# Optimization experiments

Measured on AMD Instinct MI355X. Metric: run time of the kernel, lower is better.

Reference implementation:

```python
import jax, jax.numpy as jnp
import numpy as np

D_MODEL = 512
KEY_DIM = 128
TEMP = 30.0          # RelationUnit temperature
EPS = 1e-5           # InstanceL2Norm eps
SCALE = float(np.sqrt(1.0 / (D_MODEL * 4 * 4)))  # norm_scale in layers


def _sine_pos(hw, d, dtype=jnp.float32):
    # pos_seq = ones(hw).cumsum() -> 1..hw; outer with inv_freq; cat(sin, cos)
    pos = jnp.arange(1, hw + 1, dtype=dtype)
    inv_freq = 1.0 / (10000.0 ** (jnp.arange(0, d, 2, dtype=dtype) / d))
    ang = pos[:, None] * inv_freq[None, :]          # [hw, d/2]
    return jnp.concatenate([jnp.sin(ang), jnp.cos(ang)], axis=-1)  # [hw, d]


def _attn(q, k, v, wk, bk):
    # Single-head RelationUnit: shared WK projection, L2-normalize, temp softmax, raw value.
    # q: [Lq,B,D], k,v: [Lk,B,D]
    pq = q @ wk.T + bk
    pq = pq / jnp.maximum(jnp.linalg.norm(pq, axis=-1, keepdims=True), 1e-12)
    pk = k @ wk.T + bk
    pk = pk / jnp.maximum(jnp.linalg.norm(pk, axis=-1, keepdims=True), 1e-12)
    logits = jnp.einsum('qbe,kbe->bqk', pq, pk) * TEMP   # [B,Lq,Lk]
    a = jax.nn.softmax(logits, axis=-1)
    return jnp.einsum('bqk,kbd->qbd', a, v)


def _inorm(x, ni, b, d, h, w):
    # InstanceL2Norm (size_average=True) over (d,h,w) per (ni,b) sample.
    y = x.reshape(ni, h, w, b, d)
    ss = jnp.sum(y * y, axis=(1, 2, 4), keepdims=True)
    y = y * (SCALE * jnp.sqrt((d * h * w) / (ss + EPS)))
    return y.reshape(ni * h * w, b, d)


def _flatten(x5):
    # (ni,b,d,h,w) -> (ni*h*w, b, d), matching torch view/permute/reshape order.
    ni, b, d, h, w = x5.shape
    return x5.reshape(ni, b, d, h * w).transpose(0, 3, 1, 2).reshape(ni * h * w, b, d)


def _encoder(src5, pos5, wk, bk):
    ni, b, d, h, w = src5.shape
    x = _flatten(src5) + _flatten(pos5) * 1e-3
    x = x + _attn(x, x, x, wk, bk)
    return _inorm(x, ni, b, d, h, w)


def _decoder_one(tgt5, pos5, memory, pos, wk_s, bk_s, wk_c, bk_c):
    # Single decoder layer on one image (ni == 1).
    ni, b, d, h, w = tgt5.shape
    x = _flatten(tgt5) + _flatten(pos5) * 1e-3
    x = x + _attn(x, x, x, wk_s, bk_s)
    x = _inorm(x, ni, b, d, h, w)
    mask = _attn(x, memory, pos, wk_c, bk_c)
    t2 = _inorm(x * mask, ni, b, d, h, w)
    t3 = _attn(x, memory, memory * pos, wk_c, bk_c)
    t4 = _inorm(x + t3, ni, b, d, h, w)
    x = _inorm(t2 + t4, ni, b, d, h, w)
    return x.reshape(ni, h, w, b, d).transpose(0, 3, 4, 1, 2).reshape(ni * b, d, h, w)


def _forward(train_feat, test_feat, train_label, wk_self, bk_self, wk_cross, bk_cross):
    ntr, b, d, h, w = train_feat.shape
    nte = test_feat.shape[0]
    # Sinusoidal position embedding, reshaped to (d,h,w), broadcast over imgs/batch.
    pe = _sine_pos(h * w, d, train_feat.dtype).reshape(h, w, d).transpose(2, 0, 1)
    train_pos = jnp.broadcast_to(pe, (ntr, b, d, h, w))
    test_pos = jnp.broadcast_to(pe, (nte, b, d, h, w))
    memory = _encoder(train_feat, train_pos, wk_self, bk_self)   # [ntr*h*w, b, d]
    # label -> pos value sequence [ntr*h*w, b, d] (repeated over channel dim)
    pos = train_label.reshape(ntr, b, 1, h * w).transpose(0, 3, 1, 2).reshape(ntr * h * w, b, 1)
    pos = jnp.broadcast_to(pos, (ntr * h * w, b, d))

    def dec(t4, p4):
        return _decoder_one(t4[None], p4[None], memory, pos,
                            wk_self, bk_self, wk_cross, bk_cross)

    enc_feat = jax.vmap(dec)(train_feat, train_pos).reshape(ntr * b, d, h, w)
    dec_feat = jax.vmap(dec)(test_feat, test_pos).reshape(nte * b, d, h, w)
    return enc_feat, dec_feat


def setup_inputs() -> dict:
    key = jax.random.key(0)
    k1, k2, k3, k4, k5 = jax.random.split(key, 5)
    NTR, NTE, B, D, H, W = 3, 3, 16, 512, 22, 22
    std = float(np.sqrt(2.0 / D))  # kaiming-like init for WK
    return {
        'train_feat': jax.random.normal(k1, (NTR, B, D, H, W), jnp.float32),
        'test_feat': jax.random.normal(k2, (NTE, B, D, H, W), jnp.float32),
        'train_label': jax.random.uniform(k3, (NTR, B, H, W), jnp.float32),
        'wk_self': jax.random.normal(k4, (KEY_DIM, D), jnp.float32) * std,
        'bk_self': jnp.zeros((KEY_DIM,), jnp.float32),
        'wk_cross': jax.random.normal(k5, (KEY_DIM, D), jnp.float32) * std,
        'bk_cross': jnp.zeros((KEY_DIM,), jnp.float32),
    }


def reference(train_feat, test_feat, train_label, wk_self, bk_self, wk_cross, bk_cross):
    return _forward(train_feat, test_feat, train_label,
                    wk_self, bk_self, wk_cross, bk_cross)
```

## Files before the change

kernel.cpp:

```cpp
#include <hip/hip_runtime.h>
#include <math.h>

#define BATCH   16
#define DMODEL  512
#define EKEY    128
#define HWSZ    484
#define LENC    1452
#define LKPAD   1536
#define IMG_ELEMS (HWSZ*BATCH*DMODEL)
#define ENC_OUT   11894784ull
#define SQRT_TEMP 5.4772255750516611f
#define INORM_SCALE 0.011048543456039806f
#define NEGBIG   -3.0e38f

typedef _Float16 f16;
typedef _Float16 f16x8 __attribute__((ext_vector_type(8)));
typedef _Float16 f16x4 __attribute__((ext_vector_type(4)));
typedef float    f32x4 __attribute__((ext_vector_type(4)));

__device__ __forceinline__ f32x4 mfma16(f16x8 a, f16x8 b, f32x4 c) {
  return __builtin_amdgcn_mfma_f32_16x16x32_f16(a, b, c, 0, 0, 0);
}
__device__ __forceinline__ float inorm_coef(float ss) {
  return INORM_SCALE * sqrtf(247808.0f / (ss + 1e-5f));
}

#define BARRIER() do { asm volatile("s_waitcnt lgkmcnt(0)" ::: "memory"); \
                       __builtin_amdgcn_s_barrier();                      \
                       asm volatile("" ::: "memory"); } while (0)

__global__ void init_zero_kernel(float* __restrict__ ss) { ss[threadIdx.x] = 0.0f; }

__global__ void peT_kernel(float* __restrict__ peT) {
  const int c = blockIdx.x;
  const int cc = (c < 256) ? c : c - 256;
  const float invf = 1.0f / powf(10000.0f, (float)(2 * cc) * (1.0f / 512.0f));
  for (int p = threadIdx.x; p < HWSZ; p += blockDim.x) {
    const float ang = (float)(p + 1) * invf;
    peT[c * HWSZ + p] = (c < 256) ? sinf(ang) : cosf(ang);
  }
}

__global__ void build_labelT_kernel(const float* __restrict__ lab, float* __restrict__ labT) {
  const int g = blockIdx.x;
  if (g < 48) {
    const int im = g >> 4, b = g & 15;
    for (int p = threadIdx.x; p < HWSZ; p += blockDim.x)
      labT[(size_t)b * LKPAD + im * HWSZ + p] = lab[((size_t)im * BATCH + b) * HWSZ + p];
  } else {
    const int b = g - 48;
    for (int p = LENC + threadIdx.x; p < LKPAD; p += blockDim.x)
      labT[(size_t)b * LKPAD + p] = 0.0f;
  }
}

__global__ void cvt16_kernel(const float* __restrict__ s, f16* __restrict__ d) {
  const int i = (blockIdx.x * 256 + threadIdx.x) * 4;
  const float4 v = *(const float4*)(s + i);
  f16x4 h; h[0] = (f16)v.x; h[1] = (f16)v.y; h[2] = (f16)v.z; h[3] = (f16)v.w;
  *(f16x4*)(d + i) = h;
}

__global__ void vpad_kernel(f16* __restrict__ vt) {
  const int d = blockIdx.x, b = blockIdx.y;
  const int c = LENC + threadIdx.x;
  if (c < LKPAD) vt[((size_t)b * 512 + d) * (size_t)LKPAD + c] = (f16)0.f;
}

__global__ __launch_bounds__(256) void build_input_kernel(
    const float* __restrict__ trainf, const float* __restrict__ testf,
    const float* __restrict__ peT, int i0, float* __restrict__ xout,
    f16* __restrict__ vt, int zmul, int col_im_step, int Lkp)
{
  __shared__ float tile[32][33];
  const int tx = threadIdx.x, ty = threadIdx.y;
  const int pt = blockIdx.x * 32, ct = blockIdx.y * 32;
  const int im = blockIdx.z >> 4, b = blockIdx.z & 15;
  const int g = i0 + im;
  const float* src = (g < 3 ? trainf + (size_t)g * IMG_ELEMS
                            : testf + (size_t)(g - 3) * IMG_ELEMS)
                     + (size_t)b * (512 * 484);
  const int zv = zmul ? (im * 16 + b) : b;
  const int col0 = im * col_im_step;
#pragma unroll
  for (int j = 0; j < 4; ++j) {
    const int c = ct + ty + 8 * j, p = pt + tx;
    float val = 0.0f;
    if (p < HWSZ) {
      val = src[(size_t)c * 484 + p] + 1e-3f * peT[(size_t)c * 484 + p];
      vt[((size_t)zv * 512 + c) * (size_t)Lkp + col0 + p] = (f16)val;
    } else if (zmul) {
      vt[((size_t)zv * 512 + c) * (size_t)Lkp + col0 + p] = (f16)0.f;
    }
    tile[ty + 8 * j][tx] = val;
  }
  __syncthreads();
#pragma unroll
  for (int j = 0; j < 4; ++j) {
    const int p = pt + ty + 8 * j, c = ct + tx;
    if (p < HWSZ)
      xout[(((size_t)im * HWSZ + p) * BATCH + b) * DMODEL + c] = tile[tx][ty + 8 * j];
  }
}

__global__ __launch_bounds__(256) void v16t_mem_kernel(
    const float* __restrict__ src, const float* __restrict__ ssE, f16* __restrict__ dst)
{
  __shared__ f16 tile[32][33];
  const int tx = threadIdx.x, ty = threadIdx.y;
  const int l0 = blockIdx.x * 32, d0 = blockIdx.y * 32;
  const int b = blockIdx.z;
#pragma unroll
  for (int j = 0; j < 4; ++j) {
    const int l = l0 + ty + 8 * j;
    float v = 0.0f;
    if (l < LENC) {
      const float cf = inorm_coef(ssE[(l / 484) * 16 + b]);
      v = cf * src[((size_t)l * BATCH + b) * DMODEL + d0 + tx];
    }
    tile[ty + 8 * j][tx] = (f16)v;
  }
  __syncthreads();
#pragma unroll
  for (int j = 0; j < 4; ++j) {
    const int d = d0 + ty + 8 * j, l = l0 + tx;
    if (l < LKPAD) dst[((size_t)b * 512 + d) * (size_t)LKPAD + l] = tile[tx][ty + 8 * j];
  }
}

__global__ __launch_bounds__(256) void proj_mfma_kernel(
    const float* __restrict__ X, const f16* __restrict__ W16,
    const float* __restrict__ bias, const float* __restrict__ ssg,
    f16* __restrict__ P16, int L)
{
  __shared__ f16 Xs[64][72];
  const int t = threadIdx.x;
  const int wave = t >> 6, lane = t & 63, quad = lane >> 4, ln = lane & 15;
  const size_t row0 = (size_t)blockIdx.x * 64;

  f32x4 acc[8];
#pragma unroll
  for (int nt = 0; nt < 8; ++nt) acc[nt] = (f32x4){0.f, 0.f, 0.f, 0.f};

  const int sr = t & 63, sko = (t >> 6) * 16;
  const size_t rowg = row0 + sr;
  float cf = 1.0f;
  if (ssg) {
    const int bb = (int)(rowg & 15);
    const int gg = (int)((rowg >> 4) / 484);
    cf = inorm_coef(ssg[gg * 16 + bb]);
  }
  const float* xp = X + rowg * 512 + sko;

  for (int k0 = 0; k0 < 512; k0 += 64) {
    {
      const float4 a0 = *(const float4*)(xp + k0);
      const float4 a1 = *(const float4*)(xp + k0 + 4);
      const float4 a2 = *(const float4*)(xp + k0 + 8);
      const float4 a3 = *(const float4*)(xp + k0 + 12);
      f16x8 h0, h1;
      h0[0]=(f16)(cf*a0.x); h0[1]=(f16)(cf*a0.y); h0[2]=(f16)(cf*a0.z); h0[3]=(f16)(cf*a0.w);
      h0[4]=(f16)(cf*a1.x); h0[5]=(f16)(cf*a1.y); h0[6]=(f16)(cf*a1.z); h0[7]=(f16)(cf*a1.w);
      h1[0]=(f16)(cf*a2.x); h1[1]=(f16)(cf*a2.y); h1[2]=(f16)(cf*a2.z); h1[3]=(f16)(cf*a2.w);
      h1[4]=(f16)(cf*a3.x); h1[5]=(f16)(cf*a3.y); h1[6]=(f16)(cf*a3.z); h1[7]=(f16)(cf*a3.w);
      *(f16x8*)&Xs[sr][sko]     = h0;
      *(f16x8*)&Xs[sr][sko + 8] = h1;
    }
    __syncthreads();
#pragma unroll
    for (int ks = 0; ks < 2; ++ks) {
      const f16x8 a = *(const f16x8*)&Xs[wave * 16 + ln][ks * 32 + quad * 8];
      const f16* wp = W16 + (size_t)ln * 512 + k0 + ks * 32 + quad * 8;
#pragma unroll
      for (int nt = 0; nt < 8; ++nt) {
        const f16x8 bf = *(const f16x8*)(wp + (size_t)nt * 16 * 512);
        acc[nt] = mfma16(a, bf, acc[nt]);
      }
    }
    __syncthreads();
  }

  float bj[8];
#pragma unroll
  for (int nt = 0; nt < 8; ++nt) bj[nt] = bias[nt * 16 + ln];

  float y[8][4]; float ssq[4] = {0.f, 0.f, 0.f, 0.f};
#pragma unroll
  for (int nt = 0; nt < 8; ++nt)
#pragma unroll
    for (int r = 0; r < 4; ++r) {
      const float v = acc[nt][r] + bj[nt];
      y[nt][r] = v; ssq[r] = fmaf(v, v, ssq[r]);
    }
#pragma unroll
  for (int r = 0; r < 4; ++r) {
    ssq[r] += __shfl_xor(ssq[r], 1); ssq[r] += __shfl_xor(ssq[r], 2);
    ssq[r] += __shfl_xor(ssq[r], 4); ssq[r] += __shfl_xor(ssq[r], 8);
  }
#pragma unroll
  for (int r = 0; r < 4; ++r) {
    const float inv = SQRT_TEMP / fmaxf(sqrtf(ssq[r]), 1e-12f);
    const size_t rg = row0 + (size_t)wave * 16 + quad * 4 + r;
    const int b = (int)(rg & 15);
    const size_t lg = rg >> 4;
    const int im = (int)(lg / (size_t)L);
    const int l  = (int)(lg - (size_t)im * L);
    f16* dp = P16 + ((size_t)(im * 16 + b) * (size_t)L + l) * 128 + ln;
#pragma unroll
    for (int nt = 0; nt < 8; ++nt) dp[nt * 16] = (f16)(y[nt][r] * inv);
  }
}

template<int CROSS>
__global__ __launch_bounds__(512) void attn5_kernel(
    const f16* __restrict__ pq, const f16* __restrict__ pk, const f16* __restrict__ Vt,
    const float* __restrict__ labT, float* __restrict__ X, float* __restrict__ Vout,
    const float* __restrict__ ssIn, float* __restrict__ ssO,
    float* __restrict__ ssV_, float* __restrict__ ssUV_,
    int Lq, int Lk, int Lkp, int nqb, int pk_shared, int vt_shared)
{
  __shared__ float Ssm[64][132];
  __shared__ f16   Psm[64][136];
  __shared__ float msh[64], lsh[64], ash[64], mask_sh[64];

  const int t = threadIdx.x;
  const int wave = t >> 6, lane = t & 63, quad = lane >> 4, ln = lane & 15;

  const int id = blockIdx.x;
  const int b  = (id & 7) + 8 * ((id >> 3) & 1);
  const int jj = id >> 4;
  const int qb = jj % nqb, im = jj / nqb;
  const int q0 = qb * 64;
  const int zq = im * 16 + b;
  const int zk = pk_shared ? b : zq;
  const int zv = vt_shared ? b : zq;

  const f16* pqb = pq + (size_t)zq * Lq * 128;
  const f16* pkb = pk + (size_t)zk * Lk * 128;
  const f16* Vtb = Vt + (size_t)zv * 512 * (size_t)Lkp;
  const float* ksb = CROSS ? labT + (size_t)b * LKPAD : (const float*)0;

  f16x8 qf[4][4];
#pragma unroll
  for (int mt = 0; mt < 4; ++mt) {
    int q = q0 + mt * 16 + ln; if (q > Lq - 1) q = Lq - 1;
    const f16* qp = pqb + (size_t)q * 128 + quad * 8;
#pragma unroll
    for (int es = 0; es < 4; ++es) qf[mt][es] = *(const f16x8*)(qp + es * 32);
  }
  f16x8 kf[4];
  {
    int kn = wave * 16 + ln; if (kn > Lk - 1) kn = Lk - 1;
    const f16* kp = pkb + (size_t)kn * 128 + quad * 8;
#pragma unroll
    for (int es = 0; es < 4; ++es) kf[es] = *(const f16x8*)(kp + es * 32);
  }

  f32x4 oacc[4][4];
#pragma unroll
  for (int mt = 0; mt < 4; ++mt)
#pragma unroll
    for (int nt = 0; nt < 4; ++nt) oacc[mt][nt] = (f32x4){0.f, 0.f, 0.f, 0.f};

  if (t < 64) { msh[t] = NEGBIG; lsh[t] = 0.f; ash[t] = 0.f; }
  float msum = 0.f;
  const int qs = t >> 3, cs = t & 7;
  __syncthreads();

  const f16* vrow = Vtb + (size_t)(wave * 64 + ln) * (size_t)Lkp + quad * 8;
  const int nch = (Lk + 127) >> 7;

  for (int ch = 0; ch < nch; ++ch) {
    const int k0 = ch << 7;
    f16x8 bvA[4], bvB[4];
#pragma unroll
    for (int nt = 0; nt < 4; ++nt) {
      const f16* vpn = vrow + (size_t)nt * 16 * (size_t)Lkp + k0;
      bvA[nt] = *(const f16x8*)(vpn);
      bvB[nt] = *(const f16x8*)(vpn + 32);
    }
    float4 lv[4];
    if (CROSS) {
      const float* lp = ksb + k0 + cs * 16;
#pragma unroll
      for (int i = 0; i < 4; ++i) lv[i] = *(const float4*)(lp + i * 4);
    }
    {
      f32x4 s[4];
#pragma unroll
      for (int mt = 0; mt < 4; ++mt) s[mt] = (f32x4){0.f,0.f,0.f,0.f};
#pragma unroll
      for (int es = 0; es < 4; ++es)
#pragma unroll
        for (int mt = 0; mt < 4; ++mt)
          s[mt] = mfma16(qf[mt][es], kf[es], s[mt]);
#pragma unroll
      for (int mt = 0; mt < 4; ++mt)
#pragma unroll
        for (int r = 0; r < 4; ++r)
          Ssm[mt * 16 + quad * 4 + r][wave * 16 + ln] = s[mt][r];
    }
    if (ch + 1 < nch) {
      int kn = (ch + 1) * 128 + wave * 16 + ln; if (kn > Lk - 1) kn = Lk - 1;
      const f16* kp = pkb + (size_t)kn * 128 + quad * 8;
#pragma unroll
      for (int es = 0; es < 4; ++es) kf[es] = *(const f16x8*)(kp + es * 32);
    }
    BARRIER();
    {
      f32x4 sa[4];
#pragma unroll
      for (int i = 0; i < 4; ++i) sa[i] = *(const f32x4*)&Ssm[qs][cs * 16 + i * 4];
      const int kb = k0 + cs * 16;
      float sv[16];
#pragma unroll
      for (int i = 0; i < 4; ++i)
#pragma unroll
        for (int j = 0; j < 4; ++j)
          sv[i * 4 + j] = (kb + i * 4 + j < Lk) ? sa[i][j] : NEGBIG;
      float mx = sv[0];
#pragma unroll
      for (int j = 1; j < 16; ++j) mx = fmaxf(mx, sv[j]);
      mx = fmaxf(mx, __shfl_xor(mx, 1));
      mx = fmaxf(mx, __shfl_xor(mx, 2));
      mx = fmaxf(mx, __shfl_xor(mx, 4));
      const float mold = msh[qs];
      const float mnew = fmaxf(mold, mx);
      const float alpha = __expf(mold - mnew);
      float ps = 0.f, pm = 0.f;
      f16x8 pv0, pv1;
#pragma unroll
      for (int j = 0; j < 16; ++j) {
        float p = __expf(sv[j] - mnew);
        ps += p;
        if (CROSS) p *= lv[j >> 2][j & 3];
        pm += p;
        if (j < 8) pv0[j] = (f16)p; else pv1[j - 8] = (f16)p;
      }
      *(f16x8*)&Psm[qs][cs * 16]     = pv0;
      *(f16x8*)&Psm[qs][cs * 16 + 8] = pv1;
      ps += __shfl_xor(ps, 1); ps += __shfl_xor(ps, 2); ps += __shfl_xor(ps, 4);
      msum = msum * alpha + pm;
      if (cs == 0) { msh[qs] = mnew; lsh[qs] = lsh[qs] * alpha + ps; ash[qs] = alpha; }
    }
    BARRIER();
    {
      f16x8 bvC[4];
#pragma unroll
      for (int nt = 0; nt < 4; ++nt)
        bvC[nt] = *(const f16x8*)(vrow + (size_t)nt * 16 * (size_t)Lkp + k0 + 64);
#pragma unroll
      for (int mt = 0; mt < 4; ++mt) {
        f32x4 al;
#pragma unroll
        for (int r = 0; r < 4; ++r) al[r] = ash[mt * 16 + quad * 4 + r];
#pragma unroll
        for (int nt = 0; nt < 4; ++nt) oacc[mt][nt] *= al;
      }
      f16x8 pa[4];
#pragma unroll
      for (int mt = 0; mt < 4; ++mt) pa[mt] = *(const f16x8*)&Psm[mt * 16 + ln][quad * 8];
#pragma unroll
      for (int nt = 0; nt < 4; ++nt)
#pragma unroll
        for (int mt = 0; mt < 4; ++mt)
          oacc[mt][nt] = mfma16(pa[mt], bvA[nt], oacc[mt][nt]);
      f16x8 bvD[4];
#pragma unroll
      for (int nt = 0; nt < 4; ++nt)
        bvD[nt] = *(const f16x8*)(vrow + (size_t)nt * 16 * (size_t)Lkp + k0 + 96);
#pragma unroll
      for (int mt = 0; mt < 4; ++mt) pa[mt] = *(const f16x8*)&Psm[mt * 16 + ln][32 + quad * 8];
#pragma unroll
      for (int nt = 0; nt < 4; ++nt)
#pragma unroll
        for (int mt = 0; mt < 4; ++mt)
          oacc[mt][nt] = mfma16(pa[mt], bvB[nt], oacc[mt][nt]);
#pragma unroll
      for (int mt = 0; mt < 4; ++mt) pa[mt] = *(const f16x8*)&Psm[mt * 16 + ln][64 + quad * 8];
#pragma unroll
      for (int nt = 0; nt < 4; ++nt)
#pragma unroll
        for (int mt = 0; mt < 4; ++mt)
          oacc[mt][nt] = mfma16(pa[mt], bvC[nt], oacc[mt][nt]);
#pragma unroll
      for (int mt = 0; mt < 4; ++mt) pa[mt] = *(const f16x8*)&Psm[mt * 16 + ln][96 + quad * 8];
#pragma unroll
      for (int nt = 0; nt < 4; ++nt)
#pragma unroll
        for (int mt = 0; mt < 4; ++mt)
          oacc[mt][nt] = mfma16(pa[mt], bvD[nt], oacc[mt][nt]);
    }
  }

  if (CROSS) {
    float ms = msum;
    ms += __shfl_xor(ms, 1); ms += __shfl_xor(ms, 2); ms += __shfl_xor(ms, 4);
    if (cs == 0) mask_sh[qs] = ms / lsh[qs];
    __syncthreads();
  }

  const int g0  = (im * Lq + q0) / 484;
  const int bhi = (g0 + 1) * 484 - im * Lq;
  const bool strad = (!CROSS) && (bhi < Lq) && (bhi < q0 + 64);

  float a0 = 0.f, a1 = 0.f, a2 = 0.f;
  const float cfA = CROSS ? inorm_coef(ssIn[im * 16 + b]) : 0.f;

#pragma unroll
  for (int mt = 0; mt < 4; ++mt) {
    f32x4 li;
#pragma unroll
    for (int r = 0; r < 4; ++r) li[r] = 1.0f / lsh[mt * 16 + quad * 4 + r];
#pragma unroll
    for (int r = 0; r < 4; ++r) {
      const int q = q0 + mt * 16 + quad * 4 + r;
      if (q < Lq) {
        const size_t base = (((size_t)(im * Lq + q)) * BATCH + b) * DMODEL + wave * 64 + ln;
        if (!CROSS) {
          const bool hi = (q >= bhi);
#pragma unroll
          for (int nt = 0; nt < 4; ++nt) {
            const float y = X[base + nt * 16] + oacc[mt][nt][r] * li[r];
            X[base + nt * 16] = y;
            if (hi) a1 += y * y; else a0 += y * y;
          }
        } else {
          const float mval = mask_sh[mt * 16 + quad * 4 + r];
#pragma unroll
          for (int nt = 0; nt < 4; ++nt) {
            const float x1 = cfA * X[base + nt * 16];
            const float u = x1 * mval;
            const float v = x1 + oacc[mt][nt][r] * li[r];
            X[base + nt * 16] = u;
            Vout[base + nt * 16] = v;
            a0 += u * u; a1 += v * v; a2 += u * v;
          }
        }
      }
    }
  }
#pragma unroll
  for (int m = 32; m; m >>= 1) {
    a0 += __shfl_xor(a0, m); a1 += __shfl_xor(a1, m);
    if (CROSS) a2 += __shfl_xor(a2, m);
  }
  if (lane == 0) {
    if (!CROSS) {
      atomicAdd(ssO + g0 * 16 + b, a0);
      if (strad) atomicAdd(ssO + (g0 + 1) * 16 + b, a1);
    } else {
      const int g = im * 16 + b;
      atomicAdd(ssO + g, a0);
      atomicAdd(ssV_ + g, a1);
      atomicAdd(ssUV_ + g, a2);
    }
  }
}

__global__ void coef_final_kernel(const float* __restrict__ ssU, const float* __restrict__ ssV,
                                  const float* __restrict__ ssUV, float* __restrict__ AB, int n)
{
  const int t = threadIdx.x;
  if (t < n) {
    const float su = ssU[t], sv = ssV[t], suv = ssUV[t];
    const float cu = inorm_coef(su), cv = inorm_coef(sv);
    const float ssz = cu * cu * su + cv * cv * sv + 2.f * cu * cv * suv;
    const float cz = inorm_coef(ssz);
    AB[2 * t] = cu * cz; AB[2 * t + 1] = cv * cz;
  }
}

__global__ __launch_bounds__(256) void final_out_kernel(
    const float* __restrict__ u, const float* __restrict__ v,
    const float* __restrict__ AB, float* __restrict__ out, int i0)
{
  __shared__ float tile[32][33];
  const int tx = threadIdx.x, ty = threadIdx.y;
  const int pt = blockIdx.x * 32, ct = blockIdx.y * 32;
  const int z = blockIdx.z;
  const int im = z >> 4, b = z & 15;
  const float A = AB[2 * z], B = AB[2 * z + 1];
#pragma unroll
  for (int j = 0; j < 4; ++j) {
    const int p = pt + ty + 8 * j, c = ct + tx;
    float val = 0.0f;
    if (p < HWSZ) {
      const size_t idx = (((size_t)im * HWSZ + p) * BATCH + b) * DMODEL + c;
      val = A * u[idx] + B * v[idx];
    }
    tile[ty + 8 * j][tx] = val;
  }
  __syncthreads();
  const int g = i0 + im;
  const size_t base = (g < 3 ? 0ull : ENC_OUT)
                    + ((size_t)(((g < 3 ? g : g - 3) * 16 + b) * 512)) * 484ull;
#pragma unroll
  for (int j = 0; j < 4; ++j) {
    const int c = ct + ty + 8 * j, p = pt + tx;
    if (p < HWSZ) out[base + (size_t)c * 484 + p] = tile[tx][ty + 8 * j];
  }
}

extern "C" void kernel_launch(void* const* d_in, const int* in_sizes, int n_in,
                              void* d_out, int out_size, void* d_ws, size_t ws_size,
                              hipStream_t stream) {
  (void)in_sizes; (void)n_in; (void)out_size;
  const float* train_feat  = (const float*)d_in[0];
  const float* test_feat   = (const float*)d_in[1];
  const float* train_label = (const float*)d_in[2];
  const float* wk_self     = (const float*)d_in[3];
  const float* bk_self     = (const float*)d_in[4];
  const float* wk_cross    = (const float*)d_in[5];
  const float* bk_cross    = (const float*)d_in[6];
  float* out = (float*)d_out;
  char* wsb  = (char*)d_ws;

  size_t off = 0;
  auto alloc = [&](size_t bytes) { size_t r = off; off = (r + bytes + 255) & ~(size_t)255; return r; };
  const size_t o_peT   = alloc(991232ull);
  const size_t o_labT  = alloc(16ull * LKPAD * 4);
  const size_t o_ss    = alloc(4096);
  const size_t o_w16s  = alloc(131072);
  const size_t o_w16c  = alloc(131072);
  const size_t o_xenc  = alloc(47579136ull);
  const size_t o_p16   = alloc(5947392ull);
  const size_t o_vte   = alloc(16ull*512*LKPAD*2);
  const size_t o_vtm   = alloc(16ull*512*LKPAD*2);
  const size_t fixed = off;

  float* peT  = (float*)(wsb + o_peT);
  float* labT = (float*)(wsb + o_labT);
  float* ss   = (float*)(wsb + o_ss);
  f16*   w16s = (f16*)(wsb + o_w16s);
  f16*   w16c = (f16*)(wsb + o_w16c);
  float* xenc = (float*)(wsb + o_xenc);
  f16*   p16  = (f16*)(wsb + o_p16);
  f16*   vte  = (f16*)(wsb + o_vte);
  f16*   vtm  = (f16*)(wsb + o_vtm);
  float* ssE = ss, *ssA = ss + 128, *ssU = ss + 256, *ssV = ss + 384, *ssUV = ss + 512;
  float* AB  = ss + 640;

  const size_t decPer = 15859712ull * 2 + 1982464ull + 8388608ull;
  int NB = 6;
  if (fixed + (size_t)NB * decPer + 4096 > ws_size) NB = 3;
  if (fixed + (size_t)NB * decPer + 4096 > ws_size) NB = 1;

  float* xd    = (float*)(wsb + fixed);
  float* vbuf  = xd + (size_t)NB * IMG_ELEMS;
  f16*   pq16d = (f16*)(vbuf + (size_t)NB * IMG_ELEMS);
  f16*   vtd   = pq16d + (size_t)NB * 991232ull;

  init_zero_kernel<<<dim3(1), dim3(1024), 0, stream>>>(ss);
  peT_kernel<<<dim3(512), dim3(256), 0, stream>>>(peT);
  build_labelT_kernel<<<dim3(64), dim3(256), 0, stream>>>(train_label, labT);
  cvt16_kernel<<<dim3(64), dim3(256), 0, stream>>>(wk_self, w16s);
  cvt16_kernel<<<dim3(64), dim3(256), 0, stream>>>(wk_cross, w16c);
  vpad_kernel<<<dim3(512, 16), dim3(96), 0, stream>>>(vte);

  build_input_kernel<<<dim3(16, 16, 48), dim3(32, 8), 0, stream>>>(
      train_feat, test_feat, peT, 0, xenc, vte, 0, 484, LKPAD);
  proj_mfma_kernel<<<dim3(363), dim3(256), 0, stream>>>(xenc, w16s, bk_self, (const float*)0, p16, LENC);
  attn5_kernel<0><<<dim3(23 * 16), dim3(512), 0, stream>>>(
      p16, p16, vte, (const float*)0, xenc, (float*)0, (const float*)0,
      ssE, (float*)0, (float*)0, LENC, LENC, LKPAD, 23, 0, 0);
  proj_mfma_kernel<<<dim3(363), dim3(256), 0, stream>>>(xenc, w16c, bk_cross, ssE, p16, LENC);
  v16t_mem_kernel<<<dim3(48, 16, 16), dim3(32, 8), 0, stream>>>(xenc, ssE, vtm);

  for (int i0 = 0; i0 < 6; i0 += NB) {
    build_input_kernel<<<dim3(16, 16, NB * 16), dim3(32, 8), 0, stream>>>(
        train_feat, test_feat, peT, i0, xd, vtd, 1, 0, 512);
    proj_mfma_kernel<<<dim3(NB * 121), dim3(256), 0, stream>>>(xd, w16s, bk_self, (const float*)0, pq16d, HWSZ);
    attn5_kernel<0><<<dim3(8 * 16 * NB), dim3(512), 0, stream>>>(
        pq16d, pq16d, vtd, (const float*)0, xd, (float*)0, (const float*)0,
        ssA + i0 * 16, (float*)0, (float*)0, HWSZ, HWSZ, 512, 8, 0, 0);
    proj_mfma_kernel<<<dim3(NB * 121), dim3(256), 0, stream>>>(xd, w16c, bk_cross, ssA + i0 * 16, pq16d, HWSZ);
    attn5_kernel<1><<<dim3(8 * 16 * NB), dim3(512), 0, stream>>>(
        pq16d, p16 , vtm, labT, xd, vbuf, ssA + i0 * 16,
        ssU + i0 * 16, ssV + i0 * 16, ssUV + i0 * 16, HWSZ, LENC, LKPAD, 8, 1, 1);
    coef_final_kernel<<<dim3(1), dim3(128), 0, stream>>>(
        ssU + i0 * 16, ssV + i0 * 16, ssUV + i0 * 16, AB + i0 * 32, NB * 16);
    final_out_kernel<<<dim3(16, 16, NB * 16), dim3(32, 8), 0, stream>>>(
        xd, vbuf, AB + i0 * 32, out, i0);
  }
}
```

Baseline: 1.090 ms.

## Store Q/K/V and weights in MFMA fragment-tiled layout for contiguous lane loads

```diff
diff --git a/kernel.cpp b/kernel.cpp
--- a/kernel.cpp
+++ b/kernel.cpp
@@ -29,6 +29,11 @@
                        __builtin_amdgcn_s_barrier();                      \
                        asm volatile("" ::: "memory"); } while (0)
 
+__device__ __forceinline__ size_t vfrag_addr(size_t z, int nkt, int d, int k) {
+  return (((z * 32 + (d >> 4)) * (size_t)nkt + (k >> 5)) << 9)
+         + (((k >> 3) & 3) << 7) + ((d & 15) << 3) + (k & 7);
+}
+
 __global__ void init_zero_kernel(float* __restrict__ ss) { ss[threadIdx.x] = 0.0f; }
 
 __global__ void peT_kernel(float* __restrict__ peT) {
@@ -56,21 +61,24 @@
 
 __global__ void cvt16_kernel(const float* __restrict__ s, f16* __restrict__ d) {
   const int i = (blockIdx.x * 256 + threadIdx.x) * 4;
+  const int r = i >> 9, c = i & 511;
   const float4 v = *(const float4*)(s + i);
   f16x4 h; h[0] = (f16)v.x; h[1] = (f16)v.y; h[2] = (f16)v.z; h[3] = (f16)v.w;
-  *(f16x4*)(d + i) = h;
+  f16* dp = d + ((((size_t)(r >> 4) << 4) + (c >> 5)) << 9)
+              + (((c >> 3) & 3) << 7) + ((r & 15) << 3) + (c & 7);
+  *(f16x4*)dp = h;
 }
 
 __global__ void vpad_kernel(f16* __restrict__ vt) {
   const int d = blockIdx.x, b = blockIdx.y;
-  const int c = LENC + threadIdx.x;
-  if (c < LKPAD) vt[((size_t)b * 512 + d) * (size_t)LKPAD + c] = (f16)0.f;
+  const int k = LENC + threadIdx.x;
+  if (k < LKPAD) vt[vfrag_addr(b, 48, d, k)] = (f16)0.f;
 }
 
 __global__ __launch_bounds__(256) void build_input_kernel(
     const float* __restrict__ trainf, const float* __restrict__ testf,
     const float* __restrict__ peT, int i0, float* __restrict__ xout,
-    f16* __restrict__ vt, int zmul, int col_im_step, int Lkp)
+    f16* __restrict__ vt, int zmul, int col_im_step, int nkt)
 {
   __shared__ float tile[32][33];
   const int tx = threadIdx.x, ty = threadIdx.y;
@@ -85,12 +93,13 @@
 #pragma unroll
   for (int j = 0; j < 4; ++j) {
     const int c = ct + ty + 8 * j, p = pt + tx;
+    const int k = col0 + p;
     float val = 0.0f;
     if (p < HWSZ) {
       val = src[(size_t)c * 484 + p] + 1e-3f * peT[(size_t)c * 484 + p];
-      vt[((size_t)zv * 512 + c) * (size_t)Lkp + col0 + p] = (f16)val;
+      vt[vfrag_addr(zv, nkt, c, k)] = (f16)val;
     } else if (zmul) {
-      vt[((size_t)zv * 512 + c) * (size_t)Lkp + col0 + p] = (f16)0.f;
+      vt[vfrag_addr(zv, nkt, c, k)] = (f16)0.f;
     }
     tile[ty + 8 * j][tx] = val;
   }
@@ -124,25 +133,26 @@
 #pragma unroll
   for (int j = 0; j < 4; ++j) {
     const int d = d0 + ty + 8 * j, l = l0 + tx;
-    if (l < LKPAD) dst[((size_t)b * 512 + d) * (size_t)LKPAD + l] = tile[tx][ty + 8 * j];
+    if (l < LKPAD) dst[vfrag_addr(b, 48, d, l)] = tile[tx][ty + 8 * j];
   }
 }
 
 __global__ __launch_bounds__(256) void proj_mfma_kernel(
     const float* __restrict__ X, const f16* __restrict__ W16,
     const float* __restrict__ bias, const float* __restrict__ ssg,
-    f16* __restrict__ P16, int L)
+    f16* __restrict__ P16, int L, int NLT)
 {
   __shared__ f16 Xs[64][72];
   const int t = threadIdx.x;
   const int wave = t >> 6, lane = t & 63, quad = lane >> 4, ln = lane & 15;
+  const int lane8 = lane * 8;
   const size_t row0 = (size_t)blockIdx.x * 64;
 
   f32x4 acc[8];
 #pragma unroll
   for (int nt = 0; nt < 8; ++nt) acc[nt] = (f32x4){0.f, 0.f, 0.f, 0.f};
 
-  const int sr = t & 63, sko = (t >> 6) * 16;
+  const int sr = t >> 2, sko = (t & 3) * 16;
   const size_t rowg = row0 + sr;
   float cf = 1.0f;
   if (ssg) {
@@ -170,10 +180,10 @@
 #pragma unroll
     for (int ks = 0; ks < 2; ++ks) {
       const f16x8 a = *(const f16x8*)&Xs[wave * 16 + ln][ks * 32 + quad * 8];
-      const f16* wp = W16 + (size_t)ln * 512 + k0 + ks * 32 + quad * 8;
+      const int kt = (k0 >> 5) + ks;
 #pragma unroll
       for (int nt = 0; nt < 8; ++nt) {
-        const f16x8 bf = *(const f16x8*)(wp + (size_t)nt * 16 * 512);
+        const f16x8 bf = *(const f16x8*)(W16 + (((size_t)(nt * 16 + kt)) << 9) + lane8);
         acc[nt] = mfma16(a, bf, acc[nt]);
       }
     }
@@ -205,19 +215,20 @@
     const size_t lg = rg >> 4;
     const int im = (int)(lg / (size_t)L);
     const int l  = (int)(lg - (size_t)im * L);
-    f16* dp = P16 + ((size_t)(im * 16 + b) * (size_t)L + l) * 128 + ln;
-#pragma unroll
-    for (int nt = 0; nt < 8; ++nt) dp[nt * 16] = (f16)(y[nt][r] * inv);
+    f16* zb = P16 + (((size_t)(im * 16 + b) * NLT + (l >> 4)) << 11) + ((l & 15) << 3) + (ln & 7);
+#pragma unroll
+    for (int nt = 0; nt < 8; ++nt)
+      zb[((size_t)(nt >> 1) << 9) + (((nt * 2 + (ln >> 3)) & 3) << 7)] = (f16)(y[nt][r] * inv);
   }
 }
 
 template<int CROSS>
-__global__ __launch_bounds__(512) void attn5_kernel(
+__global__ __launch_bounds__(512) void attn6_kernel(
     const f16* __restrict__ pq, const f16* __restrict__ pk, const f16* __restrict__ Vt,
     const float* __restrict__ labT, float* __restrict__ X, float* __restrict__ Vout,
     const float* __restrict__ ssIn, float* __restrict__ ssO,
     float* __restrict__ ssV_, float* __restrict__ ssUV_,
-    int Lq, int Lk, int Lkp, int nqb, int pk_shared, int vt_shared)
+    int Lq, int Lk, int nqb, int nltq, int nltk, int nktv, int pk_shared, int vt_shared)
 {
   __shared__ float Ssm[64][132];
   __shared__ f16   Psm[64][136];
@@ -225,6 +236,7 @@
 
   const int t = threadIdx.x;
   const int wave = t >> 6, lane = t & 63, quad = lane >> 4, ln = lane & 15;
+  const int lane8 = lane * 8;
 
   const int id = blockIdx.x;
   const int b  = (id & 7) + 8 * ((id >> 3) & 1);
@@ -235,25 +247,23 @@
   const int zk = pk_shared ? b : zq;
   const int zv = vt_shared ? b : zq;
 
-  const f16* pqb = pq + (size_t)zq * Lq * 128;
-  const f16* pkb = pk + (size_t)zk * Lk * 128;
-  const f16* Vtb = Vt + (size_t)zv * 512 * (size_t)Lkp;
+  const f16* pqz = pq + (((size_t)zq * nltq) << 11);
+  const f16* pkz = pk + (((size_t)zk * nltk) << 11);
+  const f16* Vw  = Vt + ((((size_t)zv * 32 + wave * 4) * (size_t)nktv) << 9) + lane8;
   const float* ksb = CROSS ? labT + (size_t)b * LKPAD : (const float*)0;
 
   f16x8 qf[4][4];
 #pragma unroll
   for (int mt = 0; mt < 4; ++mt) {
-    int q = q0 + mt * 16 + ln; if (q > Lq - 1) q = Lq - 1;
-    const f16* qp = pqb + (size_t)q * 128 + quad * 8;
-#pragma unroll
-    for (int es = 0; es < 4; ++es) qf[mt][es] = *(const f16x8*)(qp + es * 32);
+    const f16* qp = pqz + (((size_t)((q0 >> 4) + mt)) << 11) + lane8;
+#pragma unroll
+    for (int es = 0; es < 4; ++es) qf[mt][es] = *(const f16x8*)(qp + es * 512);
   }
   f16x8 kf[4];
   {
-    int kn = wave * 16 + ln; if (kn > Lk - 1) kn = Lk - 1;
-    const f16* kp = pkb + (size_t)kn * 128 + quad * 8;
-#pragma unroll
-    for (int es = 0; es < 4; ++es) kf[es] = *(const f16x8*)(kp + es * 32);
+    const f16* kp = pkz + (((size_t)wave) << 11) + lane8;
+#pragma unroll
+    for (int es = 0; es < 4; ++es) kf[es] = *(const f16x8*)(kp + es * 512);
   }
 
   f32x4 oacc[4][4];
@@ -267,17 +277,17 @@
   const int qs = t >> 3, cs = t & 7;
   __syncthreads();
 
-  const f16* vrow = Vtb + (size_t)(wave * 64 + ln) * (size_t)Lkp + quad * 8;
   const int nch = (Lk + 127) >> 7;
 
   for (int ch = 0; ch < nch; ++ch) {
     const int k0 = ch << 7;
+    const int ktb = k0 >> 5;
     f16x8 bvA[4], bvB[4];
 #pragma unroll
     for (int nt = 0; nt < 4; ++nt) {
-      const f16* vpn = vrow + (size_t)nt * 16 * (size_t)Lkp + k0;
+      const f16* vpn = Vw + (((size_t)nt * nktv + ktb) << 9);
       bvA[nt] = *(const f16x8*)(vpn);
-      bvB[nt] = *(const f16x8*)(vpn + 32);
+      bvB[nt] = *(const f16x8*)(vpn + 512);
     }
     float4 lv[4];
     if (CROSS) {
@@ -301,10 +311,9 @@
           Ssm[mt * 16 + quad * 4 + r][wave * 16 + ln] = s[mt][r];
     }
     if (ch + 1 < nch) {
-      int kn = (ch + 1) * 128 + wave * 16 + ln; if (kn > Lk - 1) kn = Lk - 1;
-      const f16* kp = pkb + (size_t)kn * 128 + quad * 8;
-#pragma unroll
-      for (int es = 0; es < 4; ++es) kf[es] = *(const f16x8*)(kp + es * 32);
+      const f16* kp = pkz + (((size_t)(((ch + 1) << 3) + wave)) << 11) + lane8;
+#pragma unroll
+      for (int es = 0; es < 4; ++es) kf[es] = *(const f16x8*)(kp + es * 512);
     }
     BARRIER();
     {
@@ -348,7 +357,7 @@
       f16x8 bvC[4];
 #pragma unroll
       for (int nt = 0; nt < 4; ++nt)
-        bvC[nt] = *(const f16x8*)(vrow + (size_t)nt * 16 * (size_t)Lkp + k0 + 64);
+        bvC[nt] = *(const f16x8*)(Vw + (((size_t)nt * nktv + ktb + 2) << 9));
 #pragma unroll
       for (int mt = 0; mt < 4; ++mt) {
         f32x4 al;
@@ -368,7 +377,7 @@
       f16x8 bvD[4];
 #pragma unroll
       for (int nt = 0; nt < 4; ++nt)
-        bvD[nt] = *(const f16x8*)(vrow + (size_t)nt * 16 * (size_t)Lkp + k0 + 96);
+        bvD[nt] = *(const f16x8*)(Vw + (((size_t)nt * nktv + ktb + 3) << 9));
 #pragma unroll
       for (int mt = 0; mt < 4; ++mt) pa[mt] = *(const f16x8*)&Psm[mt * 16 + ln][32 + quad * 8];
 #pragma unroll
@@ -524,7 +533,7 @@
   const size_t o_w16s  = alloc(131072);
   const size_t o_w16c  = alloc(131072);
   const size_t o_xenc  = alloc(47579136ull);
-  const size_t o_p16   = alloc(5947392ull);
+  const size_t o_p16   = alloc(6291456ull);
   const size_t o_vte   = alloc(16ull*512*LKPAD*2);
   const size_t o_vtm   = alloc(16ull*512*LKPAD*2);
   const size_t fixed = off;
@@ -541,7 +550,7 @@
   float* ssE = ss, *ssA = ss + 128, *ssU = ss + 256, *ssV = ss + 384, *ssUV = ss + 512;
   float* AB  = ss + 640;
 
-  const size_t decPer = 15859712ull * 2 + 1982464ull + 8388608ull;
+  const size_t decPer = 15859712ull * 2 + 2097152ull + 8388608ull;
   int NB = 6;
   if (fixed + (size_t)NB * decPer + 4096 > ws_size) NB = 3;
   if (fixed + (size_t)NB * decPer + 4096 > ws_size) NB = 1;
@@ -549,7 +558,7 @@
   float* xd    = (float*)(wsb + fixed);
   float* vbuf  = xd + (size_t)NB * IMG_ELEMS;
   f16*   pq16d = (f16*)(vbuf + (size_t)NB * IMG_ELEMS);
-  f16*   vtd   = pq16d + (size_t)NB * 991232ull;
+  f16*   vtd   = pq16d + (size_t)NB * 1048576ull;
 
   init_zero_kernel<<<dim3(1), dim3(1024), 0, stream>>>(ss);
   peT_kernel<<<dim3(512), dim3(256), 0, stream>>>(peT);
@@ -559,25 +568,25 @@
   vpad_kernel<<<dim3(512, 16), dim3(96), 0, stream>>>(vte);
 
   build_input_kernel<<<dim3(16, 16, 48), dim3(32, 8), 0, stream>>>(
-      train_feat, test_feat, peT, 0, xenc, vte, 0, 484, LKPAD);
-  proj_mfma_kernel<<<dim3(363), dim3(256), 0, stream>>>(xenc, w16s, bk_self, (const float*)0, p16, LENC);
-  attn5_kernel<0><<<dim3(23 * 16), dim3(512), 0, stream>>>(
+      train_feat, test_feat, peT, 0, xenc, vte, 0, 484, 48);
+  proj_mfma_kernel<<<dim3(363), dim3(256), 0, stream>>>(xenc, w16s, bk_self, (const float*)0, p16, LENC, 96);
+  attn6_kernel<0><<<dim3(23 * 16), dim3(512), 0, stream>>>(
       p16, p16, vte, (const float*)0, xenc, (float*)0, (const float*)0,
-      ssE, (float*)0, (float*)0, LENC, LENC, LKPAD, 23, 0, 0);
-  proj_mfma_kernel<<<dim3(363), dim3(256), 0, stream>>>(xenc, w16c, bk_cross, ssE, p16, LENC);
+      ssE, (float*)0, (float*)0, LENC, LENC, 23, 96, 96, 48, 0, 0);
+  proj_mfma_kernel<<<dim3(363), dim3(256), 0, stream>>>(xenc, w16c, bk_cross, ssE, p16, LENC, 96);
   v16t_mem_kernel<<<dim3(48, 16, 16), dim3(32, 8), 0, stream>>>(xenc, ssE, vtm);
 
   for (int i0 = 0; i0 < 6; i0 += NB) {
     build_input_kernel<<<dim3(16, 16, NB * 16), dim3(32, 8), 0, stream>>>(
-        train_feat, test_feat, peT, i0, xd, vtd, 1, 0, 512);
-    proj_mfma_kernel<<<dim3(NB * 121), dim3(256), 0, stream>>>(xd, w16s, bk_self, (const float*)0, pq16d, HWSZ);
-    attn5_kernel<0><<<dim3(8 * 16 * NB), dim3(512), 0, stream>>>(
+        train_feat, test_feat, peT, i0, xd, vtd, 1, 0, 16);
+    proj_mfma_kernel<<<dim3(NB * 121), dim3(256), 0, stream>>>(xd, w16s, bk_self, (const float*)0, pq16d, HWSZ, 32);
+    attn6_kernel<0><<<dim3(8 * 16 * NB), dim3(512), 0, stream>>>(
         pq16d, pq16d, vtd, (const float*)0, xd, (float*)0, (const float*)0,
-        ssA + i0 * 16, (float*)0, (float*)0, HWSZ, HWSZ, 512, 8, 0, 0);
-    proj_mfma_kernel<<<dim3(NB * 121), dim3(256), 0, stream>>>(xd, w16c, bk_cross, ssA + i0 * 16, pq16d, HWSZ);
-    attn5_kernel<1><<<dim3(8 * 16 * NB), dim3(512), 0, stream>>>(
+        ssA + i0 * 16, (float*)0, (float*)0, HWSZ, HWSZ, 8, 32, 32, 16, 0, 0);
+    proj_mfma_kernel<<<dim3(NB * 121), dim3(256), 0, stream>>>(xd, w16c, bk_cross, ssA + i0 * 16, pq16d, HWSZ, 32);
+    attn6_kernel<1><<<dim3(8 * 16 * NB), dim3(512), 0, stream>>>(
         pq16d, p16 , vtm, labT, xd, vbuf, ssA + i0 * 16,
-        ssU + i0 * 16, ssV + i0 * 16, ssUV + i0 * 16, HWSZ, LENC, LKPAD, 8, 1, 1);
+        ssU + i0 * 16, ssV + i0 * 16, ssUV + i0 * 16, HWSZ, LENC, 8, 32, 96, 48, 1, 1);
     coef_final_kernel<<<dim3(1), dim3(128), 0, stream>>>(
         ssU + i0 * 16, ssV + i0 * 16, ssUV + i0 * 16, AB + i0 * 32, NB * 16);
     final_out_kernel<<<dim3(16, 16, NB * 16), dim3(32, 8), 0, stream>>>(
```

New measurement: 916.7 us. 1.19x faster.
